# Kernel tuning notes

Hardware: AMD Instinct MI355X
Metric: run time of the kernel (lower is better)

## Reference

```python
import jax, jax.numpy as jnp
import numpy as np

B, T, C = 16, 4096, 2048
H = 16
HS = C // H  # 128
SCALE = 1.0 / float(np.sqrt(HS))


def setup_inputs() -> dict:
    key = jax.random.key(0)
    k1, k2, k3, k4, k5 = jax.random.split(key, 5)
    x = jax.random.normal(k1, (B, 1, C), dtype=jnp.float32)
    k = jax.random.normal(k2, (B, H, T, HS), dtype=jnp.float32)
    v = jax.random.normal(k3, (B, H, T, HS), dtype=jnp.float32)
    # nn.Linear(dim, dim, bias=False) weights, applied as x @ W.T
    Wq = jax.random.normal(k4, (C, C), dtype=jnp.float32) * (1.0 / np.sqrt(C))
    Wp = jax.random.normal(k5, (C, C), dtype=jnp.float32) * (1.0 / np.sqrt(C))
    return {"x": x, "k": k, "v": v, "Wq": Wq, "Wp": Wp}


def reference(x, k, v, Wq, Wp):
    # decode branch: only last token of x is used
    q = x[:, -1, :] @ Wq.T                      # [B, C]
    q = q.reshape(B, H, HS)                     # [B, H, HS] (single query token)
    # att = (q * k).sum(-1) * scale  -> scores over cache length T
    att = jnp.einsum('bhd,bhtd->bht', q, k) * SCALE   # [B, H, T]
    att = jax.nn.softmax(att, axis=-1)
    # y = att @ v  -> [B, H, 1, HS], collapsed here
    y = jnp.einsum('bht,bhtd->bhd', att, v)     # [B, H, HS]
    y = y.reshape(B, 1, C)                      # transpose(1,2).view(B,1,C) equivalent for 1 token
    out = y @ Wp.T                              # [B, 1, C]; dropout is identity in eval
    return out
```

## Files before the change

### kernel.cpp

```cpp
#include <hip/hip_runtime.h>
#include <cmath>

#define C_DIM 2048
#define B_DIM 16
#define H_DIM 16
#define HS_DIM 128
#define T_DIM 4096
#define ATT_SCALE 0.08838834764831845f
#define TCHUNK 512
#define NCHUNK (T_DIM / TCHUNK)

__global__ __launch_bounds__(256) void gemv16_kernel(
    const float* __restrict__ X, const float* __restrict__ W,
    float* __restrict__ O) {
  const int lane = threadIdx.x & 63;
  const int wave = threadIdx.x >> 6;
  const int n = blockIdx.x * 4 + wave;
  const float* wrow = W + (size_t)n * C_DIM;

  float acc[B_DIM];
#pragma unroll
  for (int m = 0; m < B_DIM; ++m) acc[m] = 0.f;

#pragma unroll
  for (int i = 0; i < C_DIM / 256; ++i) {
    const int j = i * 256 + lane * 4;
    const float4 w4 = *reinterpret_cast<const float4*>(wrow + j);
#pragma unroll
    for (int m = 0; m < B_DIM; ++m) {
      const float4 x4 = *reinterpret_cast<const float4*>(X + m * C_DIM + j);
      acc[m] += w4.x * x4.x + w4.y * x4.y + w4.z * x4.z + w4.w * x4.w;
    }
  }

#pragma unroll
  for (int m = 0; m < B_DIM; ++m) {
#pragma unroll
    for (int mask = 32; mask >= 1; mask >>= 1)
      acc[m] += __shfl_xor(acc[m], mask, 64);
  }
  if (lane == 0) {
#pragma unroll
    for (int m = 0; m < B_DIM; ++m) O[(size_t)m * C_DIM + n] = acc[m];
  }
}

__global__ __launch_bounds__(256, 6) void attn_partial_kernel(
    const float* __restrict__ q, const float* __restrict__ k,
    const float* __restrict__ v, float* __restrict__ pm,
    float* __restrict__ pl, float* __restrict__ py) {
  const int blk = blockIdx.x;
  const int bh = blk >> 3;
  const int chunk = blk & 7;
  const int lane = threadIdx.x & 63;
  const int wave = threadIdx.x >> 6;
  const int half = lane >> 5;
  const int dl = lane & 31;
  const int unit = wave * 2 + half;

  const float4* kp = reinterpret_cast<const float4*>(k + (size_t)bh * T_DIM * HS_DIM);
  const float4* vp = reinterpret_cast<const float4*>(v + (size_t)bh * T_DIM * HS_DIM);
  const float4 qv = reinterpret_cast<const float4*>(q + (size_t)bh * HS_DIM)[dl];

  float m = -INFINITY, l = 0.f;
  float y0 = 0.f, y1 = 0.f, y2 = 0.f, y3 = 0.f;
  const int tbase = chunk * TCHUNK + unit;

#pragma unroll 4
  for (int ti = 0; ti < TCHUNK / 8; ++ti) {
    const int t = tbase + ti * 8;
    const float4 kv = kp[(size_t)t * 32 + dl];
    const float4 vv = vp[(size_t)t * 32 + dl];
    float p = kv.x * qv.x + kv.y * qv.y + kv.z * qv.z + kv.w * qv.w;
#pragma unroll
    for (int mask = 16; mask >= 1; mask >>= 1) p += __shfl_xor(p, mask, 64);
    const float s = p * ATT_SCALE;
    const float mn = fmaxf(m, s);
    const float c = __expf(m - mn);
    const float e = __expf(s - mn);
    l = l * c + e;
    y0 = fmaf(y0, c, e * vv.x);
    y1 = fmaf(y1, c, e * vv.y);
    y2 = fmaf(y2, c, e * vv.z);
    y3 = fmaf(y3, c, e * vv.w);
    m = mn;
  }

  __shared__ float lm[8];
  __shared__ float ll[8];
  __shared__ float ly[8 * HS_DIM];
  reinterpret_cast<float4*>(ly)[unit * 32 + dl] = make_float4(y0, y1, y2, y3);
  if (dl == 0) { lm[unit] = m; ll[unit] = l; }
  __syncthreads();

  const int tid = threadIdx.x;
  if (tid < HS_DIM) {
    float gm = lm[0];
#pragma unroll
    for (int u = 1; u < 8; ++u) gm = fmaxf(gm, lm[u]);
    float L = 0.f, yd = 0.f;
#pragma unroll
    for (int u = 0; u < 8; ++u) {
      const float e = __expf(lm[u] - gm);
      L = fmaf(e, ll[u], L);
      yd = fmaf(e, ly[u * HS_DIM + tid], yd);
    }
    py[(size_t)blk * HS_DIM + tid] = yd;
    if (tid == 0) { pm[blk] = gm; pl[blk] = L; }
  }
}

__global__ __launch_bounds__(128) void attn_combine_kernel(
    const float* __restrict__ pm, const float* __restrict__ pl,
    const float* __restrict__ py, float* __restrict__ y) {
  const int bh = blockIdx.x;
  const int d = threadIdx.x;
  float gm = -INFINITY;
#pragma unroll
  for (int c = 0; c < NCHUNK; ++c) gm = fmaxf(gm, pm[bh * NCHUNK + c]);
  float L = 0.f, yd = 0.f;
#pragma unroll
  for (int c = 0; c < NCHUNK; ++c) {
    const float e = __expf(pm[bh * NCHUNK + c] - gm);
    L = fmaf(e, pl[bh * NCHUNK + c], L);
    yd = fmaf(e, py[(size_t)(bh * NCHUNK + c) * HS_DIM + d], yd);
  }
  y[(size_t)bh * HS_DIM + d] = yd / L;
}

extern "C" void kernel_launch(void* const* d_in, const int* in_sizes, int n_in,
                              void* d_out, int out_size, void* d_ws, size_t ws_size,
                              hipStream_t stream) {
  const float* x  = (const float*)d_in[0];
  const float* k  = (const float*)d_in[1];
  const float* v  = (const float*)d_in[2];
  const float* Wq = (const float*)d_in[3];
  const float* Wp = (const float*)d_in[4];
  float* out = (float*)d_out;

  float* ws   = (float*)d_ws;
  float* q_ws = ws;
  float* y_ws = ws + B_DIM * C_DIM;
  float* pm   = y_ws + B_DIM * C_DIM;
  float* pl   = pm + B_DIM * H_DIM * NCHUNK;
  float* py   = pl + B_DIM * H_DIM * NCHUNK;

  hipLaunchKernelGGL(gemv16_kernel, dim3(C_DIM / 4), dim3(256), 0, stream,
                     x, Wq, q_ws);
  hipLaunchKernelGGL(attn_partial_kernel, dim3(B_DIM * H_DIM * NCHUNK), dim3(256), 0, stream,
                     q_ws, k, v, pm, pl, py);
  hipLaunchKernelGGL(attn_combine_kernel, dim3(B_DIM * H_DIM), dim3(128), 0, stream,
                     pm, pl, py, y_ws);
  hipLaunchKernelGGL(gemv16_kernel, dim3(C_DIM / 4), dim3(256), 0, stream,
                     y_ws, Wp, out);
}
```

Baseline: 280.3 us.

## Split fused online-softmax attention into scores, stats and PV passes

```diff
diff --git a/kernel.cpp b/kernel.cpp
--- a/kernel.cpp
+++ b/kernel.cpp
@@ -7,8 +7,8 @@
 #define HS_DIM 128
 #define T_DIM 4096
 #define ATT_SCALE 0.08838834764831845f
-#define TCHUNK 512
-#define NCHUNK (T_DIM / TCHUNK)
+#define ROWS_PER_BLK 256
+#define NCHUNK (T_DIM / ROWS_PER_BLK)
 
 __global__ __launch_bounds__(256) void gemv16_kernel(
     const float* __restrict__ X, const float* __restrict__ W,
@@ -45,13 +45,12 @@
   }
 }
 
-__global__ __launch_bounds__(256, 6) void attn_partial_kernel(
+__global__ __launch_bounds__(256) void attn_scores_kernel(
     const float* __restrict__ q, const float* __restrict__ k,
-    const float* __restrict__ v, float* __restrict__ pm,
-    float* __restrict__ pl, float* __restrict__ py) {
+    float* __restrict__ s) {
   const int blk = blockIdx.x;
-  const int bh = blk >> 3;
-  const int chunk = blk & 7;
+  const int bh = blk >> 4;
+  const int chunk = blk & 15;
   const int lane = threadIdx.x & 63;
   const int wave = threadIdx.x >> 6;
   const int half = lane >> 5;
@@ -59,73 +58,112 @@
   const int unit = wave * 2 + half;
 
   const float4* kp = reinterpret_cast<const float4*>(k + (size_t)bh * T_DIM * HS_DIM);
-  const float4* vp = reinterpret_cast<const float4*>(v + (size_t)bh * T_DIM * HS_DIM);
   const float4 qv = reinterpret_cast<const float4*>(q + (size_t)bh * HS_DIM)[dl];
+  const int tbase = chunk * ROWS_PER_BLK + unit;
 
-  float m = -INFINITY, l = 0.f;
-  float y0 = 0.f, y1 = 0.f, y2 = 0.f, y3 = 0.f;
-  const int tbase = chunk * TCHUNK + unit;
-
-#pragma unroll 4
-  for (int ti = 0; ti < TCHUNK / 8; ++ti) {
+#pragma unroll 8
+  for (int ti = 0; ti < ROWS_PER_BLK / 8; ++ti) {
     const int t = tbase + ti * 8;
     const float4 kv = kp[(size_t)t * 32 + dl];
-    const float4 vv = vp[(size_t)t * 32 + dl];
     float p = kv.x * qv.x + kv.y * qv.y + kv.z * qv.z + kv.w * qv.w;
 #pragma unroll
     for (int mask = 16; mask >= 1; mask >>= 1) p += __shfl_xor(p, mask, 64);
-    const float s = p * ATT_SCALE;
-    const float mn = fmaxf(m, s);
-    const float c = __expf(m - mn);
-    const float e = __expf(s - mn);
-    l = l * c + e;
-    y0 = fmaf(y0, c, e * vv.x);
-    y1 = fmaf(y1, c, e * vv.y);
-    y2 = fmaf(y2, c, e * vv.z);
-    y3 = fmaf(y3, c, e * vv.w);
-    m = mn;
+    if (dl == 0) s[(size_t)bh * T_DIM + t] = p * ATT_SCALE;
+  }
+}
+
+__global__ __launch_bounds__(256) void attn_stats_kernel(
+    const float* __restrict__ s, float* __restrict__ mg,
+    float* __restrict__ lg) {
+  const int bh = blockIdx.x;
+  const int tid = threadIdx.x;
+  const int lane = tid & 63;
+  const int wave = tid >> 6;
+  const float4* sp = reinterpret_cast<const float4*>(s + (size_t)bh * T_DIM);
+
+  float4 vv[4];
+  float mx = -INFINITY;
+#pragma unroll
+  for (int i = 0; i < 4; ++i) {
+    vv[i] = sp[i * 256 + tid];
+    mx = fmaxf(mx, fmaxf(fmaxf(vv[i].x, vv[i].y), fmaxf(vv[i].z, vv[i].w)));
+  }
+#pragma unroll
+  for (int mask = 32; mask >= 1; mask >>= 1)
+    mx = fmaxf(mx, __shfl_xor(mx, mask, 64));
+
+  __shared__ float redm[4];
+  __shared__ float redl[4];
+  if (lane == 0) redm[wave] = mx;
+  __syncthreads();
+  const float gm = fmaxf(fmaxf(redm[0], redm[1]), fmaxf(redm[2], redm[3]));
+
+  float sum = 0.f;
+#pragma unroll
+  for (int i = 0; i < 4; ++i) {
+    sum += __expf(vv[i].x - gm) + __expf(vv[i].y - gm) +
+           __expf(vv[i].z - gm) + __expf(vv[i].w - gm);
+  }
+#pragma unroll
+  for (int mask = 32; mask >= 1; mask >>= 1) sum += __shfl_xor(sum, mask, 64);
+  if (lane == 0) redl[wave] = sum;
+  __syncthreads();
+  if (tid == 0) {
+    mg[bh] = gm;
+    lg[bh] = redl[0] + redl[1] + redl[2] + redl[3];
+  }
+}
+
+__global__ __launch_bounds__(256) void attn_pv_kernel(
+    const float* __restrict__ s, const float* __restrict__ mg,
+    const float* __restrict__ v, float* __restrict__ py) {
+  const int blk = blockIdx.x;
+  const int bh = blk >> 4;
+  const int chunk = blk & 15;
+  const int lane = threadIdx.x & 63;
+  const int wave = threadIdx.x >> 6;
+  const int half = lane >> 5;
+  const int dl = lane & 31;
+  const int unit = wave * 2 + half;
+
+  const float4* vp = reinterpret_cast<const float4*>(v + (size_t)bh * T_DIM * HS_DIM);
+  const float gm = mg[bh];
+  const int tbase = chunk * ROWS_PER_BLK + unit;
+
+  float y0 = 0.f, y1 = 0.f, y2 = 0.f, y3 = 0.f;
+#pragma unroll 8
+  for (int ti = 0; ti < ROWS_PER_BLK / 8; ++ti) {
+    const int t = tbase + ti * 8;
+    const float4 vv = vp[(size_t)t * 32 + dl];
+    const float p = __expf(s[(size_t)bh * T_DIM + t] - gm);
+    y0 = fmaf(p, vv.x, y0);
+    y1 = fmaf(p, vv.y, y1);
+    y2 = fmaf(p, vv.z, y2);
+    y3 = fmaf(p, vv.w, y3);
   }
 
-  __shared__ float lm[8];
-  __shared__ float ll[8];
   __shared__ float ly[8 * HS_DIM];
   reinterpret_cast<float4*>(ly)[unit * 32 + dl] = make_float4(y0, y1, y2, y3);
-  if (dl == 0) { lm[unit] = m; ll[unit] = l; }
   __syncthreads();
-
   const int tid = threadIdx.x;
   if (tid < HS_DIM) {
-    float gm = lm[0];
+    float acc = 0.f;
 #pragma unroll
-    for (int u = 1; u < 8; ++u) gm = fmaxf(gm, lm[u]);
-    float L = 0.f, yd = 0.f;
-#pragma unroll
-    for (int u = 0; u < 8; ++u) {
-      const float e = __expf(lm[u] - gm);
-      L = fmaf(e, ll[u], L);
-      yd = fmaf(e, ly[u * HS_DIM + tid], yd);
-    }
-    py[(size_t)blk * HS_DIM + tid] = yd;
-    if (tid == 0) { pm[blk] = gm; pl[blk] = L; }
+    for (int u = 0; u < 8; ++u) acc += ly[u * HS_DIM + tid];
+    py[(size_t)blk * HS_DIM + tid] = acc;
   }
 }
 
 __global__ __launch_bounds__(128) void attn_combine_kernel(
-    const float* __restrict__ pm, const float* __restrict__ pl,
-    const float* __restrict__ py, float* __restrict__ y) {
+    const float* __restrict__ py, const float* __restrict__ lg,
+    float* __restrict__ y) {
   const int bh = blockIdx.x;
   const int d = threadIdx.x;
-  float gm = -INFINITY;
+  float acc = 0.f;
 #pragma unroll
-  for (int c = 0; c < NCHUNK; ++c) gm = fmaxf(gm, pm[bh * NCHUNK + c]);
-  float L = 0.f, yd = 0.f;
-#pragma unroll
-  for (int c = 0; c < NCHUNK; ++c) {
-    const float e = __expf(pm[bh * NCHUNK + c] - gm);
-    L = fmaf(e, pl[bh * NCHUNK + c], L);
-    yd = fmaf(e, py[(size_t)(bh * NCHUNK + c) * HS_DIM + d], yd);
-  }
-  y[(size_t)bh * HS_DIM + d] = yd / L;
+  for (int c = 0; c < NCHUNK; ++c)
+    acc += py[((size_t)bh * NCHUNK + c) * HS_DIM + d];
+  y[(size_t)bh * HS_DIM + d] = acc / lg[bh];
 }
 
 extern "C" void kernel_launch(void* const* d_in, const int* in_sizes, int n_in,
@@ -140,17 +178,22 @@
 
   float* ws   = (float*)d_ws;
   float* q_ws = ws;
-  float* y_ws = ws + B_DIM * C_DIM;
-  float* pm   = y_ws + B_DIM * C_DIM;
-  float* pl   = pm + B_DIM * H_DIM * NCHUNK;
-  float* py   = pl + B_DIM * H_DIM * NCHUNK;
+  float* y_ws = q_ws + B_DIM * C_DIM;
+  float* s_ws = y_ws + B_DIM * C_DIM;
+  float* m_ws = s_ws + (size_t)B_DIM * H_DIM * T_DIM;
+  float* l_ws = m_ws + B_DIM * H_DIM;
+  float* py_ws = l_ws + B_DIM * H_DIM;
 
   hipLaunchKernelGGL(gemv16_kernel, dim3(C_DIM / 4), dim3(256), 0, stream,
                      x, Wq, q_ws);
-  hipLaunchKernelGGL(attn_partial_kernel, dim3(B_DIM * H_DIM * NCHUNK), dim3(256), 0, stream,
-                     q_ws, k, v, pm, pl, py);
+  hipLaunchKernelGGL(attn_scores_kernel, dim3(B_DIM * H_DIM * NCHUNK), dim3(256), 0, stream,
+                     q_ws, k, s_ws);
+  hipLaunchKernelGGL(attn_stats_kernel, dim3(B_DIM * H_DIM), dim3(256), 0, stream,
+                     s_ws, m_ws, l_ws);
+  hipLaunchKernelGGL(attn_pv_kernel, dim3(B_DIM * H_DIM * NCHUNK), dim3(256), 0, stream,
+                     s_ws, m_ws, v, py_ws);
   hipLaunchKernelGGL(attn_combine_kernel, dim3(B_DIM * H_DIM), dim3(128), 0, stream,
-                     pm, pl, py, y_ws);
+                     py_ws, l_ws, y_ws);
   hipLaunchKernelGGL(gemv16_kernel, dim3(C_DIM / 4), dim3(256), 0, stream,
                      y_ws, Wp, out);
 }
```

Measured after the change: 290.3 us. 1.04x slower.
